# Optimization experiments

Measured on AMD Instinct MI355X. Metric: run time of the kernel, lower is better.

Reference implementation:

```python
import jax, jax.numpy as jnp
import numpy as np

LN_EPS = 1e-10


def _log_g(x):
    # log of g(x) where g(x) = x + 0.5 for x >= 0 else sigmoid(x)
    return jnp.where(x >= 0, jnp.log(jax.nn.relu(x) + 0.5), -jax.nn.softplus(-x))


def setup_inputs() -> dict:
    key = jax.random.key(0)
    k1, k2 = jax.random.split(key)
    B, T, D, H = 8, 4096, 512, 512
    x = jax.random.normal(k1, (B, T, D), dtype=jnp.float32)
    ln_gamma = jnp.ones((D,), dtype=jnp.float32)
    ln_beta = jnp.zeros((D,), dtype=jnp.float32)
    W_gh = jax.random.normal(k2, (D, 2 * H), dtype=jnp.float32) * 0.02
    return {"x": x, "ln_gamma": ln_gamma, "ln_beta": ln_beta, "W_gh": W_gh}


def reference(x, ln_gamma, ln_beta, W_gh):
    # LayerNorm over last dim
    mu = jnp.mean(x, axis=-1, keepdims=True)
    var = jnp.mean(jnp.square(x - mu), axis=-1, keepdims=True)
    xn = (x - mu) * jax.lax.rsqrt(var + LN_EPS) * ln_gamma + ln_beta

    # minGRU projection: gate logits k and candidate pre-activation
    gh = jnp.einsum('btd,dh->bth', xn, W_gh)  # [B, T, 2H]
    H = W_gh.shape[1] // 2
    k_gate, h_pre = gh[..., :H], gh[..., H:]

    # log-space parallel scan (Heinsen): h_t = (1-z_t) h_{t-1} + z_t g(h_pre_t)
    log_z = -jax.nn.softplus(-k_gate)        # log sigmoid(k)
    log_coeffs = -jax.nn.softplus(k_gate)    # log(1 - sigmoid(k))
    log_values = log_z + _log_g(h_pre)

    a_star = jnp.cumsum(log_coeffs, axis=1)
    log_h = a_star + jax.lax.cumlogsumexp(log_values - a_star, axis=1)
    h = jnp.exp(log_h)  # [B, T, H]

    # residual (res_proj is Identity since input_size == hidden_size)
    out = h + x
    hidden = h[:, -1]  # last hidden state [B, H]
    return out, hidden
```

## Files before the change

kernel.cpp:

```cpp
#include <hip/hip_runtime.h>
#include <stdint.h>

#define NB 8
#define NT 4096
#define ND 512
#define NH 512
#define NN 1024
#define NM (NB * NT)
#define NK 512
#define NCH 128
#define CTS 32

typedef __bf16 bf16x8 __attribute__((ext_vector_type(8)));
typedef float floatx4 __attribute__((ext_vector_type(4)));
typedef unsigned int uint_g __attribute__((address_space(1)));
typedef unsigned int uint_l __attribute__((address_space(3)));

__device__ __forceinline__ float bf2f(unsigned short u) {
    union { unsigned int i; float f; } v; v.i = ((unsigned int)u) << 16; return v.f;
}
__device__ __forceinline__ unsigned short f2bf(float f) {
    union { float f; unsigned int i; } v; v.f = f;
    return (unsigned short)((v.i + 0x7FFFu + ((v.i >> 16) & 1u)) >> 16);
}

__device__ __forceinline__ void load_lds16(const void* g, void* l) {
    __builtin_amdgcn_global_load_lds((const uint_g*)g, (uint_l*)l, 16, 0, 0);
}

__global__ __launch_bounds__(256) void ln_kernel(const float* __restrict__ x,
                                                 const float* __restrict__ gamma,
                                                 const float* __restrict__ beta,
                                                 unsigned short* __restrict__ xn) {
    int wid = threadIdx.x >> 6, lane = threadIdx.x & 63;
    size_t row = (size_t)blockIdx.x * 4 + wid;
    const float4* xr = (const float4*)(x + row * ND);
    float4 v0 = xr[lane];
    float4 v1 = xr[lane + 64];
    float s  = (v0.x + v0.y) + (v0.z + v0.w) + (v1.x + v1.y) + (v1.z + v1.w);
    float sq = v0.x * v0.x + v0.y * v0.y + v0.z * v0.z + v0.w * v0.w
             + v1.x * v1.x + v1.y * v1.y + v1.z * v1.z + v1.w * v1.w;
#pragma unroll
    for (int off = 32; off > 0; off >>= 1) {
        s  += __shfl_xor(s,  off, 64);
        sq += __shfl_xor(sq, off, 64);
    }
    float mu   = s * (1.0f / ND);
    float var  = sq * (1.0f / ND) - mu * mu;
    float rstd = rsqrtf(var + 1e-10f);
    const float4* gr = (const float4*)gamma;
    const float4* br = (const float4*)beta;
    float4 g0 = gr[lane], g1 = gr[lane + 64];
    float4 b0 = br[lane], b1 = br[lane + 64];
    ushort4 o0, o1;
    o0.x = f2bf((v0.x - mu) * rstd * g0.x + b0.x);
    o0.y = f2bf((v0.y - mu) * rstd * g0.y + b0.y);
    o0.z = f2bf((v0.z - mu) * rstd * g0.z + b0.z);
    o0.w = f2bf((v0.w - mu) * rstd * g0.w + b0.w);
    o1.x = f2bf((v1.x - mu) * rstd * g1.x + b1.x);
    o1.y = f2bf((v1.y - mu) * rstd * g1.y + b1.y);
    o1.z = f2bf((v1.z - mu) * rstd * g1.z + b1.z);
    o1.w = f2bf((v1.w - mu) * rstd * g1.w + b1.w);
    ushort4* xo = (ushort4*)(xn + row * ND);
    xo[lane]      = o0;
    xo[lane + 64] = o1;
}

__global__ __launch_bounds__(256) void wt_kernel(const float* __restrict__ W,
                                                 unsigned short* __restrict__ Wt) {
    __shared__ float tile[32][33];
    int n0 = blockIdx.x * 32;
    int k0 = blockIdx.y * 32;
    int tx = threadIdx.x, ty = threadIdx.y;
#pragma unroll
    for (int j = 0; j < 4; ++j)
        tile[ty + j * 8][tx] = W[(size_t)(k0 + ty + j * 8) * NN + n0 + tx];
    __syncthreads();
#pragma unroll
    for (int j = 0; j < 4; ++j)
        Wt[(size_t)(n0 + ty + j * 8) * NK + k0 + tx] = f2bf(tile[tx][ty + j * 8]);
}

__global__ __launch_bounds__(256) void gemm_kernel(const unsigned short* __restrict__ A,
                                                   const unsigned short* __restrict__ Bt,
                                                   unsigned short* __restrict__ C) {
    __shared__ __align__(16) unsigned short As[128 * 64];
    __shared__ __align__(16) unsigned short Bs[128 * 64];
    int tid  = threadIdx.x;
    int lane = tid & 63;
    int wid  = tid >> 6;
    int wm = wid & 1, wn = wid >> 1;
    int bx = blockIdx.x;
    int nt = bx & 7;
    int mt = bx >> 3;
    const int Rm = mt * 128, Rn = nt * 128;

    int rloc = lane >> 3;
    int cl   = lane & 7;
    int cg   = cl ^ rloc;

    int frow = lane & 15;
    int quad = lane >> 4;
    int fx   = lane & 7;

    floatx4 acc[4][4];
#pragma unroll
    for (int i = 0; i < 4; ++i)
#pragma unroll
        for (int j = 0; j < 4; ++j)
            acc[i][j] = (floatx4){0.f, 0.f, 0.f, 0.f};

#pragma unroll 1
    for (int kt = 0; kt < NK / 64; ++kt) {
        int k0 = kt * 64;
        __syncthreads();
#pragma unroll
        for (int s = 0; s < 4; ++s) {
            int g  = wid * 4 + s;
            int ml = g * 8 + rloc;
            load_lds16(A + (size_t)(Rm + ml) * NK + k0 + cg * 8, As + g * 512);
        }
#pragma unroll
        for (int s = 0; s < 4; ++s) {
            int g  = wid * 4 + s;
            int nl = g * 8 + rloc;
            load_lds16(Bt + (size_t)(Rn + nl) * NK + k0 + cg * 8, Bs + g * 512);
        }
        __syncthreads();
#pragma unroll
        for (int ks = 0; ks < 2; ++ks) {
            int ch = (ks * 4 + quad) ^ fx;
            bf16x8 af[4], bfr[4];
#pragma unroll
            for (int mi = 0; mi < 4; ++mi) {
                int ml = wm * 64 + mi * 16 + frow;
                af[mi] = *(const bf16x8*)(As + ml * 64 + ch * 8);
            }
#pragma unroll
            for (int ni = 0; ni < 4; ++ni) {
                int nl = wn * 64 + ni * 16 + frow;
                bfr[ni] = *(const bf16x8*)(Bs + nl * 64 + ch * 8);
            }
#pragma unroll
            for (int mi = 0; mi < 4; ++mi)
#pragma unroll
                for (int ni = 0; ni < 4; ++ni)
                    acc[mi][ni] = __builtin_amdgcn_mfma_f32_16x16x32_bf16(
                        af[mi], bfr[ni], acc[mi][ni], 0, 0, 0);
        }
    }
#pragma unroll
    for (int mi = 0; mi < 4; ++mi)
#pragma unroll
        for (int ni = 0; ni < 4; ++ni)
#pragma unroll
            for (int r = 0; r < 4; ++r) {
                int row = Rm + wm * 64 + mi * 16 + quad * 4 + r;
                int col = Rn + wn * 64 + ni * 16 + frow;
                C[(size_t)row * NN + col] = f2bf(acc[mi][ni][r]);
            }
}

__device__ __forceinline__ void gate_av(unsigned short ku, unsigned short pu,
                                        float& a, float& v) {
    float k = bf2f(ku), p = bf2f(pu);
    float e = __expf(k);
    a = __builtin_amdgcn_rcpf(1.0f + e);
    float z = e * a;
    float gneg = __builtin_amdgcn_rcpf(1.0f + __expf(-p));
    float g = (p >= 0.0f) ? (p + 0.5f) : gneg;
    v = z * g;
}

__global__ __launch_bounds__(128) void scan1_kernel(const unsigned short* __restrict__ gh,
                                                    float* __restrict__ cA,
                                                    float* __restrict__ cV) {
    int b = blockIdx.x >> 7, c = blockIdx.x & 127;
    int h = threadIdx.x * 4;
    const unsigned short* base = gh + ((size_t)(b * NT + c * CTS)) * NN;
    float A0 = 1.f, A1 = 1.f, A2 = 1.f, A3 = 1.f;
    float V0 = 0.f, V1 = 0.f, V2 = 0.f, V3 = 0.f;
#pragma unroll 8
    for (int t = 0; t < CTS; ++t) {
        const unsigned short* p = base + (size_t)t * NN;
        ushort4 kk = *(const ushort4*)(p + h);
        ushort4 hh = *(const ushort4*)(p + NH + h);
        float a, v;
        gate_av(kk.x, hh.x, a, v); V0 = a * V0 + v; A0 *= a;
        gate_av(kk.y, hh.y, a, v); V1 = a * V1 + v; A1 *= a;
        gate_av(kk.z, hh.z, a, v); V2 = a * V2 + v; A2 *= a;
        gate_av(kk.w, hh.w, a, v); V3 = a * V3 + v; A3 *= a;
    }
    size_t o = ((size_t)b * NH + h) * NCH + c;
    cA[o] = A0; cA[o + NCH] = A1; cA[o + 2 * NCH] = A2; cA[o + 3 * NCH] = A3;
    cV[o] = V0; cV[o + NCH] = V1; cV[o + 2 * NCH] = V2; cV[o + 3 * NCH] = V3;
}

__global__ __launch_bounds__(256) void scan2_kernel(const float* __restrict__ cA,
                                                    const float* __restrict__ cV,
                                                    float* __restrict__ hinit) {
    int w = blockIdx.x * 4 + (threadIdx.x >> 6);
    int lane = threadIdx.x & 63;
    int b = w >> 9, h = w & 511;
    const float2* a2p = (const float2*)(cA + ((size_t)b * NH + h) * NCH);
    const float2* v2p = (const float2*)(cV + ((size_t)b * NH + h) * NCH);
    float2 a2 = a2p[lane];
    float2 v2 = v2p[lane];
    float A = a2.y * a2.x;
    float V = a2.y * v2.x + v2.y;
#pragma unroll
    for (int off = 1; off < 64; off <<= 1) {
        float Ap = __shfl_up(A, off, 64);
        float Vp = __shfl_up(V, off, 64);
        if (lane >= off) { V = A * Vp + V; A = A * Ap; }
    }
    float excl = __shfl_up(V, 1, 64);
    if (lane == 0) excl = 0.f;
    float e0 = excl;
    float e1 = a2.x * e0 + v2.x;
    hinit[((size_t)b * NCH + 2 * lane) * NH + h]     = e0;
    hinit[((size_t)b * NCH + 2 * lane + 1) * NH + h] = e1;
}

__global__ __launch_bounds__(128) void scan3_kernel(const unsigned short* __restrict__ gh,
                                                    const float* __restrict__ hinit,
                                                    const float* __restrict__ x,
                                                    float* __restrict__ out,
                                                    float* __restrict__ hidden) {
    int b = blockIdx.x >> 7, c = blockIdx.x & 127;
    int h = threadIdx.x * 4;
    size_t row0 = (size_t)(b * NT + c * CTS);
    const unsigned short* base = gh + row0 * NN;
    const float* xb = x + row0 * ND;
    float* ob = out + row0 * ND;
    float4 hv = *(const float4*)(hinit + ((size_t)b * NCH + c) * NH + h);
#pragma unroll 8
    for (int t = 0; t < CTS; ++t) {
        const unsigned short* p = base + (size_t)t * NN;
        ushort4 kk = *(const ushort4*)(p + h);
        ushort4 hh = *(const ushort4*)(p + NH + h);
        float a, v;
        gate_av(kk.x, hh.x, a, v); hv.x = a * hv.x + v;
        gate_av(kk.y, hh.y, a, v); hv.y = a * hv.y + v;
        gate_av(kk.z, hh.z, a, v); hv.z = a * hv.z + v;
        gate_av(kk.w, hh.w, a, v); hv.w = a * hv.w + v;
        float4 xv = *(const float4*)(xb + (size_t)t * ND + h);
        float4 ov;
        ov.x = hv.x + xv.x; ov.y = hv.y + xv.y;
        ov.z = hv.z + xv.z; ov.w = hv.w + xv.w;
        *(float4*)(ob + (size_t)t * ND + h) = ov;
    }
    if (c == NCH - 1)
        *(float4*)(hidden + (size_t)b * NH + h) = hv;
}

extern "C" void kernel_launch(void* const* d_in, const int* in_sizes, int n_in,
                              void* d_out, int out_size, void* d_ws, size_t ws_size,
                              hipStream_t stream) {
    const float* x     = (const float*)d_in[0];
    const float* gamma = (const float*)d_in[1];
    const float* beta  = (const float*)d_in[2];
    const float* W     = (const float*)d_in[3];

    float* out    = (float*)d_out;
    float* hidden = out + (size_t)NM * ND;

    char* ws = (char*)d_ws;
    unsigned short* Wt = (unsigned short*)ws;
    unsigned short* gh = (unsigned short*)(ws + (size_t)(1u << 20));
    float* cA    = (float*)(ws + (size_t)(1u << 20) + (size_t)NM * NN * 2);
    float* cV    = cA + (size_t)NB * NCH * NH;
    float* hinit = cV + (size_t)NB * NCH * NH;
    unsigned short* xn = (unsigned short*)d_out;

    wt_kernel<<<dim3(32, 16), dim3(32, 8), 0, stream>>>(W, Wt);
    ln_kernel<<<NM / 4, 256, 0, stream>>>(x, gamma, beta, xn);
    gemm_kernel<<<2048, 256, 0, stream>>>(xn, Wt, gh);
    scan1_kernel<<<NB * NCH, 128, 0, stream>>>(gh, cA, cV);
    scan2_kernel<<<1024, 256, 0, stream>>>(cA, cV, hinit);
    scan3_kernel<<<NB * NCH, 128, 0, stream>>>(gh, hinit, x, out, hidden);
}
```

Measured before the change: 231.8 us.

## Fuse three-pass chunked scan into one cooperative kernel with grid sync

```diff
diff --git a/kernel.cpp b/kernel.cpp
--- a/kernel.cpp
+++ b/kernel.cpp
@@ -1,5 +1,8 @@
 #include <hip/hip_runtime.h>
+#include <hip/hip_cooperative_groups.h>
 #include <stdint.h>
+
+namespace cg = cooperative_groups;
 
 #define NB 8
 #define NT 4096
@@ -91,8 +94,8 @@
     int wid  = tid >> 6;
     int wm = wid & 1, wn = wid >> 1;
     int bx = blockIdx.x;
-    int nt = bx & 7;
-    int mt = bx >> 3;
+    int mt = bx & 255;
+    int nt = bx >> 8;
     const int Rm = mt * 128, Rn = nt * 128;
 
     int rloc = lane >> 3;
@@ -172,12 +175,17 @@
     v = z * g;
 }
 
-__global__ __launch_bounds__(128) void scan1_kernel(const unsigned short* __restrict__ gh,
-                                                    float* __restrict__ cA,
-                                                    float* __restrict__ cV) {
+__global__ __launch_bounds__(128) void scan_fused(const unsigned short* __restrict__ gh,
+                                                  const float* __restrict__ x,
+                                                  float* __restrict__ out,
+                                                  float* __restrict__ hidden,
+                                                  float* __restrict__ cA,
+                                                  float* __restrict__ cV) {
     int b = blockIdx.x >> 7, c = blockIdx.x & 127;
     int h = threadIdx.x * 4;
-    const unsigned short* base = gh + ((size_t)(b * NT + c * CTS)) * NN;
+    size_t row0 = (size_t)(b * NT + c * CTS);
+    const unsigned short* base = gh + row0 * NN;
+
     float A0 = 1.f, A1 = 1.f, A2 = 1.f, A3 = 1.f;
     float V0 = 0.f, V1 = 0.f, V2 = 0.f, V3 = 0.f;
 #pragma unroll 8
@@ -191,49 +199,27 @@
         gate_av(kk.z, hh.z, a, v); V2 = a * V2 + v; A2 *= a;
         gate_av(kk.w, hh.w, a, v); V3 = a * V3 + v; A3 *= a;
     }
-    size_t o = ((size_t)b * NH + h) * NCH + c;
-    cA[o] = A0; cA[o + NCH] = A1; cA[o + 2 * NCH] = A2; cA[o + 3 * NCH] = A3;
-    cV[o] = V0; cV[o + NCH] = V1; cV[o + 2 * NCH] = V2; cV[o + 3 * NCH] = V3;
-}
-
-__global__ __launch_bounds__(256) void scan2_kernel(const float* __restrict__ cA,
-                                                    const float* __restrict__ cV,
-                                                    float* __restrict__ hinit) {
-    int w = blockIdx.x * 4 + (threadIdx.x >> 6);
-    int lane = threadIdx.x & 63;
-    int b = w >> 9, h = w & 511;
-    const float2* a2p = (const float2*)(cA + ((size_t)b * NH + h) * NCH);
-    const float2* v2p = (const float2*)(cV + ((size_t)b * NH + h) * NCH);
-    float2 a2 = a2p[lane];
-    float2 v2 = v2p[lane];
-    float A = a2.y * a2.x;
-    float V = a2.y * v2.x + v2.y;
-#pragma unroll
-    for (int off = 1; off < 64; off <<= 1) {
-        float Ap = __shfl_up(A, off, 64);
-        float Vp = __shfl_up(V, off, 64);
-        if (lane >= off) { V = A * Vp + V; A = A * Ap; }
-    }
-    float excl = __shfl_up(V, 1, 64);
-    if (lane == 0) excl = 0.f;
-    float e0 = excl;
-    float e1 = a2.x * e0 + v2.x;
-    hinit[((size_t)b * NCH + 2 * lane) * NH + h]     = e0;
-    hinit[((size_t)b * NCH + 2 * lane + 1) * NH + h] = e1;
-}
-
-__global__ __launch_bounds__(128) void scan3_kernel(const unsigned short* __restrict__ gh,
-                                                    const float* __restrict__ hinit,
-                                                    const float* __restrict__ x,
-                                                    float* __restrict__ out,
-                                                    float* __restrict__ hidden) {
-    int b = blockIdx.x >> 7, c = blockIdx.x & 127;
-    int h = threadIdx.x * 4;
-    size_t row0 = (size_t)(b * NT + c * CTS);
-    const unsigned short* base = gh + row0 * NN;
+    size_t o = (size_t)blockIdx.x * NH + h;
+    *(float4*)(cA + o) = make_float4(A0, A1, A2, A3);
+    *(float4*)(cV + o) = make_float4(V0, V1, V2, V3);
+
+    cg::this_grid().sync();
+
+    float4 hv = make_float4(0.f, 0.f, 0.f, 0.f);
+    const float* ap = cA + ((size_t)b * NCH) * NH + h;
+    const float* vp = cV + ((size_t)b * NCH) * NH + h;
+#pragma unroll 4
+    for (int pch = 0; pch < c; ++pch) {
+        float4 a = *(const float4*)(ap + (size_t)pch * NH);
+        float4 v = *(const float4*)(vp + (size_t)pch * NH);
+        hv.x = a.x * hv.x + v.x;
+        hv.y = a.y * hv.y + v.y;
+        hv.z = a.z * hv.z + v.z;
+        hv.w = a.w * hv.w + v.w;
+    }
+
     const float* xb = x + row0 * ND;
     float* ob = out + row0 * ND;
-    float4 hv = *(const float4*)(hinit + ((size_t)b * NCH + c) * NH + h);
 #pragma unroll 8
     for (int t = 0; t < CTS; ++t) {
         const unsigned short* p = base + (size_t)t * NN;
@@ -268,15 +254,22 @@
     char* ws = (char*)d_ws;
     unsigned short* Wt = (unsigned short*)ws;
     unsigned short* gh = (unsigned short*)(ws + (size_t)(1u << 20));
-    float* cA    = (float*)(ws + (size_t)(1u << 20) + (size_t)NM * NN * 2);
-    float* cV    = cA + (size_t)NB * NCH * NH;
-    float* hinit = cV + (size_t)NB * NCH * NH;
+    float* cA = (float*)(ws + (size_t)(1u << 20) + (size_t)NM * NN * 2);
+    float* cV = cA + (size_t)NB * NCH * NH;
     unsigned short* xn = (unsigned short*)d_out;
 
     wt_kernel<<<dim3(32, 16), dim3(32, 8), 0, stream>>>(W, Wt);
     ln_kernel<<<NM / 4, 256, 0, stream>>>(x, gamma, beta, xn);
     gemm_kernel<<<2048, 256, 0, stream>>>(xn, Wt, gh);
-    scan1_kernel<<<NB * NCH, 128, 0, stream>>>(gh, cA, cV);
-    scan2_kernel<<<1024, 256, 0, stream>>>(cA, cV, hinit);
-    scan3_kernel<<<NB * NCH, 128, 0, stream>>>(gh, hinit, x, out, hidden);
-}
+
+    const unsigned short* ghp = gh;
+    const float* xp = x;
+    float* outp = out;
+    float* hiddenp = hidden;
+    float* cAp = cA;
+    float* cVp = cV;
+    void* args[] = {(void*)&ghp, (void*)&xp, (void*)&outp,
+                    (void*)&hiddenp, (void*)&cAp, (void*)&cVp};
+    hipLaunchCooperativeKernel((void*)scan_fused, dim3(NB * NCH), dim3(128),
+                               args, 0, stream);
+}
```

New measurement: 319.5 us. 37.8% more time.
